# Performance work log

Measured on AMD Instinct MI355X. Metric: run time of the kernel, lower is better.

The kernel has to match this reference:

```python
import jax, jax.numpy as jnp
import numpy as np
import math

B, S, D = 4, 2048, 1024
H = 16
DH = D // H
NEG = -1e20


def setup_inputs() -> dict:
    key = jax.random.key(0)
    ks = jax.random.split(key, 8)
    Q_batch = jax.random.normal(ks[0], (B, S, D), dtype=jnp.float32)
    K_batch = jax.random.normal(ks[1], (B, S, D), dtype=jnp.float32)
    V_batch = jax.random.normal(ks[2], (B, S, D), dtype=jnp.float32)
    valid_lens = jax.random.randint(ks[3], (B,), 0, S).astype(jnp.int64)
    # LazyLinear weights, stored as (in, out) so projection is x @ W
    sc = 1.0 / math.sqrt(D)
    Wq = jax.random.normal(ks[4], (D, D), dtype=jnp.float32) * sc
    Wk = jax.random.normal(ks[5], (D, D), dtype=jnp.float32) * sc
    Wv = jax.random.normal(ks[6], (D, D), dtype=jnp.float32) * sc
    Wo = jax.random.normal(ks[7], (D, D), dtype=jnp.float32) * sc
    return {"Q_batch": Q_batch, "K_batch": K_batch, "V_batch": V_batch,
            "valid_lens": valid_lens, "Wq": Wq, "Wk": Wk, "Wv": Wv, "Wo": Wo}


def reference(Q_batch, K_batch, V_batch, valid_lens, Wq, Wk, Wv, Wo):
    b, nq, _ = Q_batch.shape
    nk = K_batch.shape[1]
    # project and split heads (feature dim split head-major, matching transpose_qkv)
    q = (Q_batch @ Wq).reshape(b, nq, H, DH).transpose(0, 2, 1, 3)  # (b,h,nq,dh)
    k = (K_batch @ Wk).reshape(b, nk, H, DH).transpose(0, 2, 1, 3)  # (b,h,nk,dh)
    v = (V_batch @ Wv).reshape(b, nk, H, DH).transpose(0, 2, 1, 3)  # (b,h,nk,dh)
    scores = jnp.einsum('bhqd,bhkd->bhqk', q, k) / math.sqrt(DH)
    # mask keys at position >= valid_lens[b] (shared across heads and queries)
    key_pos = jnp.arange(nk)
    mask = key_pos[None, None, None, :] < valid_lens[:, None, None, None]
    scores = jnp.where(mask, scores, NEG)
    w = jax.nn.softmax(scores, axis=-1)  # dropout rate 0 -> identity
    o = jnp.einsum('bhqk,bhkd->bhqd', w, v)           # (b,h,nq,dh)
    o = o.transpose(0, 2, 1, 3).reshape(b, nq, H * DH)  # concat heads
    return o @ Wo
```

## Files before the change

kernel.cpp:

```cpp
#include <hip/hip_runtime.h>
#include <stdint.h>

typedef unsigned short u16;
using bf16x8 = __attribute__((ext_vector_type(8))) __bf16;
using f32x4  = __attribute__((ext_vector_type(4))) float;
using u16x8  = __attribute__((ext_vector_type(8))) unsigned short;
using u16x4  = __attribute__((ext_vector_type(4))) unsigned short;

#define NH   16
#define DHD  64
#define SEQ  2048
#define DD   1024

__device__ inline u16 bfbits(float f) {
    __bf16 h = (__bf16)f;
    return __builtin_bit_cast(u16, h);
}

__device__ inline void gld16(const u16* g, u16* l) {
    __builtin_amdgcn_global_load_lds(
        (const __attribute__((address_space(1))) void*)g,
        (__attribute__((address_space(3))) void*)l,
        16, 0, 0);
}

__global__ __launch_bounds__(256) void transpose4(
    const float* __restrict__ s0, const float* __restrict__ s1,
    const float* __restrict__ s2, const float* __restrict__ s3,
    u16* __restrict__ d0, u16* __restrict__ d1,
    u16* __restrict__ d2, u16* __restrict__ d3)
{
    const float* src = s0; u16* dst = d0;
    if (blockIdx.z == 1) { src = s1; dst = d1; }
    else if (blockIdx.z == 2) { src = s2; dst = d2; }
    else if (blockIdx.z == 3) { src = s3; dst = d3; }

    __shared__ u16 tile[32][33];
    int tx = threadIdx.x, ty = threadIdx.y;
    int x = blockIdx.x * 32 + tx;
    int y0 = blockIdx.y * 32 + ty;
#pragma unroll
    for (int i = 0; i < 32; i += 8)
        tile[ty + i][tx] = bfbits(src[(size_t)(y0 + i) * DD + x]);
    __syncthreads();
    int x2 = blockIdx.y * 32 + tx;
    int y2 = blockIdx.x * 32 + ty;
#pragma unroll
    for (int i = 0; i < 32; i += 8)
        dst[(size_t)(y2 + i) * DD + x2] = tile[tx][ty + i];
}

__global__ __launch_bounds__(256) void cvt3(
    const float* __restrict__ s0, const float* __restrict__ s1,
    const float* __restrict__ s2,
    u16* __restrict__ d0, u16* __restrict__ d1, u16* __restrict__ d2,
    const int* __restrict__ vl)
{
    const float* src = s0; u16* dst = d0;
    if (blockIdx.z == 1) { src = s1; dst = d1; }
    else if (blockIdx.z == 2) { src = s2; dst = d2; }

    if (blockIdx.z != 0) {
        int r = blockIdx.x * 2;
        int v = vl[r >> 11];
        int ve = (v == 0) ? SEQ : v;
        int lim = ((ve + 127) >> 7) << 7;
        if ((r & (SEQ - 1)) >= lim) return;
    }

    size_t i = ((size_t)blockIdx.x * 256 + threadIdx.x) * 8;
    f32x4 a = *(const f32x4*)&src[i];
    f32x4 b = *(const f32x4*)&src[i + 4];
    u16x8 o;
#pragma unroll
    for (int j = 0; j < 4; ++j) { o[j] = bfbits(a[j]); o[j + 4] = bfbits(b[j]); }
    *(u16x8*)&dst[i] = o;
}

__global__ __launch_bounds__(256) void cvt1(
    const float* __restrict__ src, u16* __restrict__ dst)
{
    size_t i = ((size_t)blockIdx.x * 256 + threadIdx.x) * 8;
    f32x4 a = *(const f32x4*)&src[i];
    f32x4 b = *(const f32x4*)&src[i + 4];
    u16x8 o;
#pragma unroll
    for (int j = 0; j < 4; ++j) { o[j] = bfbits(a[j]); o[j + 4] = bfbits(b[j]); }
    *(u16x8*)&dst[i] = o;
}

template<int MODE>
__global__ __launch_bounds__(512, 4) void gemm_bt16(
    const u16* __restrict__ A0, const u16* __restrict__ A1, const u16* __restrict__ A2,
    const u16* __restrict__ B0, const u16* __restrict__ B1, const u16* __restrict__ B2,
    void* __restrict__ C0, void* __restrict__ C1, void* __restrict__ C2,
    const int* __restrict__ vl)
{
    const int K = 1024;
    const u16* A = A0; const u16* Bt = B0; void* C = C0;
    if (MODE == 3) {
        if (blockIdx.z == 1) { A = A1; Bt = B1; C = C1; }
        else if (blockIdx.z == 2) { A = A2; Bt = B2; C = C2; }
    }

    __shared__ __align__(16) u16 As[2][128 * 64];
    __shared__ __align__(16) u16 Bs[2][128 * 64];

    const int t = threadIdx.x;
    const int wave = t >> 6, lane = t & 63;
    const int l15 = lane & 15, q4 = lane >> 4;
    const int wm = (wave >> 1) * 32;
    const int wn = (wave & 1) * 64;

    const int gx = gridDim.x;
    const int nwg = gx * gridDim.y;
    int flat = blockIdx.y * gx + blockIdx.x;
    flat = (flat & 7) * (nwg >> 3) + (flat >> 3);
    const int m0 = (flat / gx) * 128, n0 = (flat % gx) * 128;

    if (MODE == 3 && blockIdx.z != 0) {
        int v = vl[m0 >> 11];
        int ve = (v == 0) ? SEQ : v;
        if ((m0 & (SEQ - 1)) >= ve) return;
    }

    const int sr = t >> 3;
    const int sg = (t & 7) ^ (sr & 7);
    const u16* gA = &A [(size_t)(m0 + sr) * K + sg * 8];
    const u16* gB = &Bt[(size_t)(n0 + sr) * K + sg * 8];
    const int ldst = sr * 64 + (t & 7) * 8;

    const int xr = (l15 & 7) * 8;

    f32x4 acc[2][4] = {};

    gld16(gA,                    &As[0][ldst]);
    gld16(gA + (size_t)64 * K,   &As[0][ldst + 4096]);
    gld16(gB,                    &Bs[0][ldst]);
    gld16(gB + (size_t)64 * K,   &Bs[0][ldst + 4096]);

    int cur = 0;
    for (int k0 = 0; k0 < K; k0 += 64) {
        __syncthreads();
        if (k0 + 64 < K) {
            const int nb = cur ^ 1;
            const size_t ko = k0 + 64;
            gld16(gA + ko,                  &As[nb][ldst]);
            gld16(gA + (size_t)64 * K + ko, &As[nb][ldst + 4096]);
            gld16(gB + ko,                  &Bs[nb][ldst]);
            gld16(gB + (size_t)64 * K + ko, &Bs[nb][ldst + 4096]);
        }

#pragma unroll
        for (int hf = 0; hf < 2; ++hf) {
            bf16x8 af[2], bfr[4];
#pragma unroll
            for (int i = 0; i < 2; ++i)
                af[i]  = *(const bf16x8*)&As[cur][(wm + i * 16 + l15) * 64 + ((hf * 32 + q4 * 8) ^ xr)];
#pragma unroll
            for (int j = 0; j < 4; ++j)
                bfr[j] = *(const bf16x8*)&Bs[cur][(wn + j * 16 + l15) * 64 + ((hf * 32 + q4 * 8) ^ xr)];
#pragma unroll
            for (int i = 0; i < 2; ++i)
#pragma unroll
                for (int j = 0; j < 4; ++j)
                    acc[i][j] = __builtin_amdgcn_mfma_f32_16x16x32_bf16(af[i], bfr[j], acc[i][j], 0, 0, 0);
        }
        cur ^= 1;
    }

    const bool vt_store = (MODE == 2) || (MODE == 3 && blockIdx.z == 2);

#pragma unroll
    for (int i = 0; i < 2; ++i) {
        int row_l = wm + i * 16 + q4 * 4;
#pragma unroll
        for (int j = 0; j < 4; ++j) {
            int col = n0 + wn + j * 16 + l15;
            if (MODE == 1) {
#pragma unroll
                for (int r = 0; r < 4; ++r) {
                    int row = m0 + row_l + r;
                    ((float*)C)[(size_t)row * DD + col] = acc[i][j][r];
                }
            } else if (vt_store) {
                int row = m0 + row_l;
                int b = row >> 11, s = row & (SEQ - 1);
                int h = col >> 6, dh = col & (DHD - 1);
                u16x4 pk;
#pragma unroll
                for (int r = 0; r < 4; ++r) pk[r] = bfbits(acc[i][j][r]);
                *(u16x4*)&((u16*)C)[(((size_t)(b * NH + h) * DHD + dh) << 11) | s] = pk;
            } else {
#pragma unroll
                for (int r = 0; r < 4; ++r) {
                    int row = m0 + row_l + r;
                    int b = row >> 11, s = row & (SEQ - 1);
                    int h = col >> 6, dh = col & (DHD - 1);
                    ((u16*)C)[(((size_t)(b * NH + h) * SEQ + s) << 6) | dh] = bfbits(acc[i][j][r]);
                }
            }
        }
    }
}

__global__ __launch_bounds__(256, 4) void attn(
    const u16* __restrict__ q_ws, const u16* __restrict__ k_ws,
    const u16* __restrict__ vT_ws, const int* __restrict__ valid_lens,
    u16* __restrict__ o_ws)
{
    const int bh = blockIdx.y;
    const int b = bh >> 4, h = bh & 15;
    const int qt = blockIdx.x;
    const int valid = valid_lens[b];
    const bool valid0 = (valid == 0);
    const int valid_eff = valid0 ? SEQ : valid;
    const int kt_n = (valid_eff + 63) >> 6;
    const float c2 = valid0 ? 0.f : 0.18033688011112042f;
    const float M2 = 17.312340490667562f;

    __shared__ __align__(16) u16 Kbuf[2][64 * 64];
    __shared__ __align__(16) u16 Vbuf[64 * 64];
    __shared__ __align__(16) u16 Ps[4][32][64];

    const int t = threadIdx.x;
    const int wave = t >> 6, lane = t & 63;
    const int l15 = lane & 15, q4 = lane >> 4;

    const size_t base  = (size_t)bh * SEQ * DHD;
    const size_t vbase = (size_t)bh * DHD * SEQ;

    const int q0 = qt * 128 + wave * 32;

    const int sr0 = wave * 16 + (lane >> 3);
    const int cg  = ((lane & 7) ^ (sr0 & 7)) * 8;
    const u16* gK = &k_ws [base  + (size_t)sr0 * DHD + cg];
    const u16* gV = &vT_ws[vbase + (size_t)sr0 * SEQ + cg];
    const int ldst = sr0 * 64 + (lane & 7) * 8;

    u16x8 ou;
#pragma unroll
    for (int j = 0; j < 8; ++j) ou[j] = 0x3F80;
    const bf16x8 ones = __builtin_bit_cast(bf16x8, ou);

    bf16x8 qf[2][2];
#pragma unroll
    for (int mi = 0; mi < 2; ++mi)
#pragma unroll
        for (int c = 0; c < 2; ++c)
            qf[mi][c] = *(const bf16x8*)&q_ws[base + (size_t)(q0 + mi * 16 + l15) * DHD + c * 32 + q4 * 8];

    f32x4 o4[2][4] = {};
    f32x4 l_acc[2] = {};

    const int swz  = (l15 & 7) * 8;

    gld16(gK,       &Kbuf[0][ldst]);
    gld16(gK + 512, &Kbuf[0][ldst + 512]);

    int cur = 0;
    for (int kt = 0; kt < kt_n; ++kt) {
        __syncthreads();
        {
            const u16* vv = gV + (size_t)kt * 64;
            gld16(vv,                   &Vbuf[ldst]);
            gld16(vv + (size_t)8 * SEQ, &Vbuf[ldst + 512]);
        }
        const bool pre = (kt + 1 < kt_n);
        if (pre) {
            const u16* kk = gK + (size_t)(kt + 1) * 64 * DHD;
            int bf = cur ^ 1;
            gld16(kk,       &Kbuf[bf][ldst]);
            gld16(kk + 512, &Kbuf[bf][ldst + 512]);
        }

        const u16* KK = Kbuf[cur];

        f32x4 s4[2][4] = {};
#pragma unroll
        for (int c = 0; c < 2; ++c)
#pragma unroll
            for (int ni = 0; ni < 4; ++ni) {
                bf16x8 kf = *(const bf16x8*)&KK[(ni * 16 + l15) * 64 + ((c * 32 + q4 * 8) ^ swz)];
#pragma unroll
                for (int mi = 0; mi < 2; ++mi)
                    s4[mi][ni] = __builtin_amdgcn_mfma_f32_16x16x32_bf16(kf, qf[mi][c], s4[mi][ni], 0, 0, 0);
            }

        const bool tile_full = valid0 || (kt * 64 + 64 <= valid_eff);
        if (tile_full) {
#pragma unroll
            for (int mi = 0; mi < 2; ++mi) {
                int qrow = mi * 16 + l15;
                int psw  = (l15 & 7) * 8;
#pragma unroll
                for (int ni = 0; ni < 4; ++ni) {
                    u16x4 pk;
#pragma unroll
                    for (int r = 0; r < 4; ++r) {
                        float p = __builtin_amdgcn_exp2f(__builtin_fmaf(s4[mi][ni][r], c2, -M2));
                        pk[r] = bfbits(p);
                    }
                    *(u16x4*)&Ps[wave][qrow][(ni * 16 + q4 * 4) ^ psw] = pk;
                }
            }
        } else {
#pragma unroll
            for (int mi = 0; mi < 2; ++mi) {
                int qrow = mi * 16 + l15;
                int psw  = (l15 & 7) * 8;
#pragma unroll
                for (int ni = 0; ni < 4; ++ni) {
                    u16x4 pk;
#pragma unroll
                    for (int r = 0; r < 4; ++r) {
                        bool ok = (kt * 64 + ni * 16 + q4 * 4 + r) < valid_eff;
                        float arg = ok ? __builtin_fmaf(s4[mi][ni][r], c2, -M2) : -1e30f;
                        pk[r] = bfbits(__builtin_amdgcn_exp2f(arg));
                    }
                    *(u16x4*)&Ps[wave][qrow][(ni * 16 + q4 * 4) ^ psw] = pk;
                }
            }
        }

        if (pre) asm volatile("s_waitcnt vmcnt(2)\n\ts_barrier" ::: "memory");
        else     asm volatile("s_waitcnt vmcnt(0)\n\ts_barrier" ::: "memory");

#pragma unroll
        for (int c = 0; c < 2; ++c) {
            bf16x8 pf[2];
#pragma unroll
            for (int mi = 0; mi < 2; ++mi) {
                pf[mi] = *(const bf16x8*)&Ps[wave][mi * 16 + l15][(c * 32 + q4 * 8) ^ ((l15 & 7) * 8)];
                l_acc[mi] = __builtin_amdgcn_mfma_f32_16x16x32_bf16(pf[mi], ones, l_acc[mi], 0, 0, 0);
            }
#pragma unroll
            for (int dt = 0; dt < 4; ++dt) {
                bf16x8 vf = *(const bf16x8*)&Vbuf[(dt * 16 + l15) * 64 + ((c * 32 + q4 * 8) ^ swz)];
#pragma unroll
                for (int mi = 0; mi < 2; ++mi)
                    o4[mi][dt] = __builtin_amdgcn_mfma_f32_16x16x32_bf16(pf[mi], vf, o4[mi][dt], 0, 0, 0);
            }
        }
        cur ^= 1;
    }

#pragma unroll
    for (int mi = 0; mi < 2; ++mi) {
        float inv[4];
#pragma unroll
        for (int r = 0; r < 4; ++r) inv[r] = 1.0f / l_acc[mi][r];
        int qrow = q0 + mi * 16 + q4 * 4;
#pragma unroll
        for (int dt = 0; dt < 4; ++dt) {
            int dh = dt * 16 + l15;
#pragma unroll
            for (int r = 0; r < 4; ++r) {
                float v = o4[mi][dt][r] * inv[r];
                o_ws[((size_t)(b * SEQ + qrow + r) << 10) | (h * DHD + dh)] = bfbits(v);
            }
        }
    }
}

extern "C" void kernel_launch(void* const* d_in, const int* in_sizes, int n_in,
                              void* d_out, int out_size, void* d_ws, size_t ws_size,
                              hipStream_t stream)
{
    (void)in_sizes; (void)n_in; (void)out_size;
    const float* Q  = (const float*)d_in[0];
    const float* Kb = (const float*)d_in[1];
    const float* V  = (const float*)d_in[2];
    const int*   vl = (const int*)d_in[3];
    const float* Wq = (const float*)d_in[4];
    const float* Wk = (const float*)d_in[5];
    const float* Wv = (const float*)d_in[6];
    const float* Wo = (const float*)d_in[7];
    float* out = (float*)d_out;

    char* ws = (char*)d_ws;
    u16* WqT   = (u16*)(ws + (size_t)0);
    u16* WkT   = (u16*)(ws + ((size_t)2 << 20));
    u16* WvT   = (u16*)(ws + ((size_t)4 << 20));
    u16* WoT   = (u16*)(ws + ((size_t)6 << 20));
    u16* q_ws  = (u16*)(ws + ((size_t)8 << 20));
    u16* k_ws  = (u16*)(ws + ((size_t)24 << 20));
    u16* vT_ws = (u16*)(ws + ((size_t)40 << 20));
    u16* o_ws  = (u16*)(ws + ((size_t)56 << 20));
    u16* Qbf   = (u16*)(ws + ((size_t)72 << 20));
    u16* Kbf   = (u16*)(ws + ((size_t)88 << 20));
    u16* Vbf   = (u16*)(ws + ((size_t)104 << 20));

    transpose4<<<dim3(32, 32, 4), dim3(32, 8), 0, stream>>>(
        Wq, Wk, Wv, Wo, WqT, WkT, WvT, WoT);

    const bool fused = ws_size >= ((size_t)120 << 20);
    if (fused) {
        cvt3<<<dim3(4096, 1, 3), 256, 0, stream>>>(Q, Kb, V, Qbf, Kbf, Vbf, vl);
        gemm_bt16<3><<<dim3(8, 64, 3), 512, 0, stream>>>(
            Qbf, Kbf, Vbf, WqT, WkT, WvT, q_ws, k_ws, vT_ws, vl);
    } else {
        cvt1<<<4096, 256, 0, stream>>>(Q, o_ws);
        gemm_bt16<0><<<dim3(8, 64), 512, 0, stream>>>(
            o_ws, nullptr, nullptr, WqT, nullptr, nullptr, q_ws, nullptr, nullptr, nullptr);
        cvt1<<<4096, 256, 0, stream>>>(Kb, o_ws);
        gemm_bt16<0><<<dim3(8, 64), 512, 0, stream>>>(
            o_ws, nullptr, nullptr, WkT, nullptr, nullptr, k_ws, nullptr, nullptr, nullptr);
        cvt1<<<4096, 256, 0, stream>>>(V, o_ws);
        gemm_bt16<2><<<dim3(8, 64), 512, 0, stream>>>(
            o_ws, nullptr, nullptr, WvT, nullptr, nullptr, vT_ws, nullptr, nullptr, nullptr);
    }

    attn<<<dim3(16, 64), 256, 0, stream>>>(q_ws, k_ws, vT_ws, vl, o_ws);

    gemm_bt16<1><<<dim3(8, 64), 512, 0, stream>>>(
        o_ws, nullptr, nullptr, WoT, nullptr, nullptr, out, nullptr, nullptr, nullptr);
}
```

Baseline: 283.2 us.

## Merge weight transpose into conversion kernel and double attention block size

Folds the four weight transposes into the input fp32-to-bf16 conversion launch as a fourth z-slice, removing one kernel launch in the fused path. The attention kernel now runs 512 threads (8 waves) per block covering 256 queries instead of 128, so each K/V tile loaded into shared memory is reused by twice as many query rows. Each thread issues one global-to-LDS load per tile instead of two, and the wait count is adjusted to match. The larger block doubles the P scratch in shared memory and halves the grid to 512 blocks, which may lower occupancy and make the load balance across varied valid lengths coarser.

```diff
diff --git a/kernel.cpp b/kernel.cpp
--- a/kernel.cpp
+++ b/kernel.cpp
@@ -24,6 +24,60 @@
         16, 0, 0);
 }
 
+__global__ __launch_bounds__(256) void prep(
+    const float* __restrict__ Q, const float* __restrict__ Kb,
+    const float* __restrict__ Vb,
+    const float* __restrict__ W0, const float* __restrict__ W1,
+    const float* __restrict__ W2, const float* __restrict__ W3,
+    u16* __restrict__ Qd, u16* __restrict__ Kd, u16* __restrict__ Vd,
+    u16* __restrict__ T0, u16* __restrict__ T1,
+    u16* __restrict__ T2, u16* __restrict__ T3,
+    const int* __restrict__ vl)
+{
+    const int z = blockIdx.z;
+    if (z == 3) {
+        const float* src = W0; u16* dst = T0;
+        int mat = blockIdx.x >> 10;
+        if (mat == 1) { src = W1; dst = T1; }
+        else if (mat == 2) { src = W2; dst = T2; }
+        else if (mat == 3) { src = W3; dst = T3; }
+        int wi = blockIdx.x & 1023;
+        int bx = wi & 31, by = wi >> 5;
+        __shared__ u16 tile[32][33];
+        int tx = threadIdx.x & 31, ty = threadIdx.x >> 5;
+        int x = bx * 32 + tx, y0 = by * 32 + ty;
+#pragma unroll
+        for (int i = 0; i < 32; i += 8)
+            tile[ty + i][tx] = bfbits(src[(size_t)(y0 + i) * DD + x]);
+        __syncthreads();
+        int x2 = by * 32 + tx, y2 = bx * 32 + ty;
+#pragma unroll
+        for (int i = 0; i < 32; i += 8)
+            dst[(size_t)(y2 + i) * DD + x2] = tile[tx][ty + i];
+        return;
+    }
+
+    const float* src = Q; u16* dst = Qd;
+    if (z == 1) { src = Kb; dst = Kd; }
+    else if (z == 2) { src = Vb; dst = Vd; }
+
+    if (z != 0) {
+        int r = blockIdx.x * 2;
+        int v = vl[r >> 11];
+        int ve = (v == 0) ? SEQ : v;
+        int lim = ((ve + 127) >> 7) << 7;
+        if ((r & (SEQ - 1)) >= lim) return;
+    }
+
+    size_t i = ((size_t)blockIdx.x * 256 + threadIdx.x) * 8;
+    f32x4 a = *(const f32x4*)&src[i];
+    f32x4 b = *(const f32x4*)&src[i + 4];
+    u16x8 o;
+#pragma unroll
+    for (int j = 0; j < 4; ++j) { o[j] = bfbits(a[j]); o[j + 4] = bfbits(b[j]); }
+    *(u16x8*)&dst[i] = o;
+}
+
 __global__ __launch_bounds__(256) void transpose4(
     const float* __restrict__ s0, const float* __restrict__ s1,
     const float* __restrict__ s2, const float* __restrict__ s3,
@@ -48,33 +102,6 @@
 #pragma unroll
     for (int i = 0; i < 32; i += 8)
         dst[(size_t)(y2 + i) * DD + x2] = tile[tx][ty + i];
-}
-
-__global__ __launch_bounds__(256) void cvt3(
-    const float* __restrict__ s0, const float* __restrict__ s1,
-    const float* __restrict__ s2,
-    u16* __restrict__ d0, u16* __restrict__ d1, u16* __restrict__ d2,
-    const int* __restrict__ vl)
-{
-    const float* src = s0; u16* dst = d0;
-    if (blockIdx.z == 1) { src = s1; dst = d1; }
-    else if (blockIdx.z == 2) { src = s2; dst = d2; }
-
-    if (blockIdx.z != 0) {
-        int r = blockIdx.x * 2;
-        int v = vl[r >> 11];
-        int ve = (v == 0) ? SEQ : v;
-        int lim = ((ve + 127) >> 7) << 7;
-        if ((r & (SEQ - 1)) >= lim) return;
-    }
-
-    size_t i = ((size_t)blockIdx.x * 256 + threadIdx.x) * 8;
-    f32x4 a = *(const f32x4*)&src[i];
-    f32x4 b = *(const f32x4*)&src[i + 4];
-    u16x8 o;
-#pragma unroll
-    for (int j = 0; j < 4; ++j) { o[j] = bfbits(a[j]); o[j + 4] = bfbits(b[j]); }
-    *(u16x8*)&dst[i] = o;
 }
 
 __global__ __launch_bounds__(256) void cvt1(
@@ -204,7 +231,7 @@
     }
 }
 
-__global__ __launch_bounds__(256, 4) void attn(
+__global__ __launch_bounds__(512, 4) void attn(
     const u16* __restrict__ q_ws, const u16* __restrict__ k_ws,
     const u16* __restrict__ vT_ws, const int* __restrict__ valid_lens,
     u16* __restrict__ o_ws)
@@ -221,7 +248,7 @@
 
     __shared__ __align__(16) u16 Kbuf[2][64 * 64];
     __shared__ __align__(16) u16 Vbuf[64 * 64];
-    __shared__ __align__(16) u16 Ps[4][32][64];
+    __shared__ __align__(16) u16 Ps[8][32][64];
 
     const int t = threadIdx.x;
     const int wave = t >> 6, lane = t & 63;
@@ -230,13 +257,13 @@
     const size_t base  = (size_t)bh * SEQ * DHD;
     const size_t vbase = (size_t)bh * DHD * SEQ;
 
-    const int q0 = qt * 128 + wave * 32;
-
-    const int sr0 = wave * 16 + (lane >> 3);
-    const int cg  = ((lane & 7) ^ (sr0 & 7)) * 8;
+    const int q0 = qt * 256 + wave * 32;
+
+    const int sr0 = t >> 3;
+    const int cg  = ((t & 7) ^ (sr0 & 7)) * 8;
     const u16* gK = &k_ws [base  + (size_t)sr0 * DHD + cg];
     const u16* gV = &vT_ws[vbase + (size_t)sr0 * SEQ + cg];
-    const int ldst = sr0 * 64 + (lane & 7) * 8;
+    const int ldst = sr0 * 64 + (t & 7) * 8;
 
     u16x8 ou;
 #pragma unroll
@@ -255,24 +282,15 @@
 
     const int swz  = (l15 & 7) * 8;
 
-    gld16(gK,       &Kbuf[0][ldst]);
-    gld16(gK + 512, &Kbuf[0][ldst + 512]);
+    gld16(gK, &Kbuf[0][ldst]);
 
     int cur = 0;
     for (int kt = 0; kt < kt_n; ++kt) {
         __syncthreads();
-        {
-            const u16* vv = gV + (size_t)kt * 64;
-            gld16(vv,                   &Vbuf[ldst]);
-            gld16(vv + (size_t)8 * SEQ, &Vbuf[ldst + 512]);
-        }
+        gld16(gV + (size_t)kt * 64, &Vbuf[ldst]);
         const bool pre = (kt + 1 < kt_n);
-        if (pre) {
-            const u16* kk = gK + (size_t)(kt + 1) * 64 * DHD;
-            int bf = cur ^ 1;
-            gld16(kk,       &Kbuf[bf][ldst]);
-            gld16(kk + 512, &Kbuf[bf][ldst + 512]);
-        }
+        if (pre)
+            gld16(gK + (size_t)(kt + 1) * 64 * DHD, &Kbuf[cur ^ 1][ldst]);
 
         const u16* KK = Kbuf[cur];
 
@@ -323,7 +341,7 @@
             }
         }
 
-        if (pre) asm volatile("s_waitcnt vmcnt(2)\n\ts_barrier" ::: "memory");
+        if (pre) asm volatile("s_waitcnt vmcnt(1)\n\ts_barrier" ::: "memory");
         else     asm volatile("s_waitcnt vmcnt(0)\n\ts_barrier" ::: "memory");
 
 #pragma unroll
@@ -391,15 +409,15 @@
     u16* Kbf   = (u16*)(ws + ((size_t)88 << 20));
     u16* Vbf   = (u16*)(ws + ((size_t)104 << 20));
 
-    transpose4<<<dim3(32, 32, 4), dim3(32, 8), 0, stream>>>(
-        Wq, Wk, Wv, Wo, WqT, WkT, WvT, WoT);
-
     const bool fused = ws_size >= ((size_t)120 << 20);
     if (fused) {
-        cvt3<<<dim3(4096, 1, 3), 256, 0, stream>>>(Q, Kb, V, Qbf, Kbf, Vbf, vl);
+        prep<<<dim3(4096, 1, 4), 256, 0, stream>>>(
+            Q, Kb, V, Wq, Wk, Wv, Wo, Qbf, Kbf, Vbf, WqT, WkT, WvT, WoT, vl);
         gemm_bt16<3><<<dim3(8, 64, 3), 512, 0, stream>>>(
             Qbf, Kbf, Vbf, WqT, WkT, WvT, q_ws, k_ws, vT_ws, vl);
     } else {
+        transpose4<<<dim3(32, 32, 4), dim3(32, 8), 0, stream>>>(
+            Wq, Wk, Wv, Wo, WqT, WkT, WvT, WoT);
         cvt1<<<4096, 256, 0, stream>>>(Q, o_ws);
         gemm_bt16<0><<<dim3(8, 64), 512, 0, stream>>>(
             o_ws, nullptr, nullptr, WqT, nullptr, nullptr, q_ws, nullptr, nullptr, nullptr);
@@ -411,7 +429,7 @@
             o_ws, nullptr, nullptr, WvT, nullptr, nullptr, vT_ws, nullptr, nullptr, nullptr);
     }
 
-    attn<<<dim3(16, 64), 256, 0, stream>>>(q_ws, k_ws, vT_ws, vl, o_ws);
+    attn<<<dim3(8, 64), 512, 0, stream>>>(q_ws, k_ws, vT_ws, vl, o_ws);
 
     gemm_bt16<1><<<dim3(8, 64), 512, 0, stream>>>(
         o_ws, nullptr, nullptr, WoT, nullptr, nullptr, out, nullptr, nullptr, nullptr);
```

Result: no change. 281.6 us (-0.6%).

## Fuse fp32-to-bf16 input conversion into the QKV projection GEMM A-tile load

Applied to the files above, without the earlier changes.

Removes the separate cvt3 pass and its bf16 staging buffers. The MODE 3 GEMM now loads fp32 activations directly into registers, converts them to bf16, and writes them into swizzled LDS after the MFMA loop, which overlaps the next tile's global loads with compute. This saves a full write and re-read of the bf16 copies, but the A operand now reads twice the bytes per tile through registers instead of direct-to-LDS loads. It also adds register pressure and sched barriers.

```diff
diff --git a/kernel.cpp b/kernel.cpp
--- a/kernel.cpp
+++ b/kernel.cpp
@@ -50,33 +50,6 @@
         dst[(size_t)(y2 + i) * DD + x2] = tile[tx][ty + i];
 }
 
-__global__ __launch_bounds__(256) void cvt3(
-    const float* __restrict__ s0, const float* __restrict__ s1,
-    const float* __restrict__ s2,
-    u16* __restrict__ d0, u16* __restrict__ d1, u16* __restrict__ d2,
-    const int* __restrict__ vl)
-{
-    const float* src = s0; u16* dst = d0;
-    if (blockIdx.z == 1) { src = s1; dst = d1; }
-    else if (blockIdx.z == 2) { src = s2; dst = d2; }
-
-    if (blockIdx.z != 0) {
-        int r = blockIdx.x * 2;
-        int v = vl[r >> 11];
-        int ve = (v == 0) ? SEQ : v;
-        int lim = ((ve + 127) >> 7) << 7;
-        if ((r & (SEQ - 1)) >= lim) return;
-    }
-
-    size_t i = ((size_t)blockIdx.x * 256 + threadIdx.x) * 8;
-    f32x4 a = *(const f32x4*)&src[i];
-    f32x4 b = *(const f32x4*)&src[i + 4];
-    u16x8 o;
-#pragma unroll
-    for (int j = 0; j < 4; ++j) { o[j] = bfbits(a[j]); o[j + 4] = bfbits(b[j]); }
-    *(u16x8*)&dst[i] = o;
-}
-
 __global__ __launch_bounds__(256) void cvt1(
     const float* __restrict__ src, u16* __restrict__ dst)
 {
@@ -96,6 +69,7 @@
     void* __restrict__ C0, void* __restrict__ C1, void* __restrict__ C2,
     const int* __restrict__ vl)
 {
+    constexpr bool ACVT = (MODE == 3);
     const int K = 1024;
     const u16* A = A0; const u16* Bt = B0; void* C = C0;
     if (MODE == 3) {
@@ -126,30 +100,60 @@
 
     const int sr = t >> 3;
     const int sg = (t & 7) ^ (sr & 7);
-    const u16* gA = &A [(size_t)(m0 + sr) * K + sg * 8];
     const u16* gB = &Bt[(size_t)(n0 + sr) * K + sg * 8];
     const int ldst = sr * 64 + (t & 7) * 8;
 
+    const int arow = t >> 2;
+    const int acol = (t & 3) * 16;
+    const int asw  = (arow & 7) * 8;
+    const float* gAf = nullptr;
+    const u16*   gA  = nullptr;
+    if constexpr (ACVT) gAf = &((const float*)A)[(size_t)(m0 + arow) * K + acol];
+    else                gA  = &A[(size_t)(m0 + sr) * K + sg * 8];
+
     const int xr = (l15 & 7) * 8;
 
     f32x4 acc[2][4] = {};
-
-    gld16(gA,                    &As[0][ldst]);
-    gld16(gA + (size_t)64 * K,   &As[0][ldst + 4096]);
-    gld16(gB,                    &Bs[0][ldst]);
-    gld16(gB + (size_t)64 * K,   &Bs[0][ldst + 4096]);
+    f32x4 ar[4];
+
+    if constexpr (ACVT) {
+#pragma unroll
+        for (int j = 0; j < 4; ++j) ar[j] = *(const f32x4*)(gAf + 4 * j);
+    } else {
+        gld16(gA,                  &As[0][ldst]);
+        gld16(gA + (size_t)64 * K, &As[0][ldst + 4096]);
+    }
+    gld16(gB,                  &Bs[0][ldst]);
+    gld16(gB + (size_t)64 * K, &Bs[0][ldst + 4096]);
+    if constexpr (ACVT) {
+        u16x8 w0, w1;
+#pragma unroll
+        for (int j = 0; j < 4; ++j) {
+            w0[j] = bfbits(ar[0][j]); w0[j + 4] = bfbits(ar[1][j]);
+            w1[j] = bfbits(ar[2][j]); w1[j + 4] = bfbits(ar[3][j]);
+        }
+        *(u16x8*)&As[0][arow * 64 + (acol ^ asw)]       = w0;
+        *(u16x8*)&As[0][arow * 64 + ((acol + 8) ^ asw)] = w1;
+    }
 
     int cur = 0;
     for (int k0 = 0; k0 < K; k0 += 64) {
         __syncthreads();
-        if (k0 + 64 < K) {
+        const bool pre = (k0 + 64 < K);
+        if (pre) {
             const int nb = cur ^ 1;
             const size_t ko = k0 + 64;
-            gld16(gA + ko,                  &As[nb][ldst]);
-            gld16(gA + (size_t)64 * K + ko, &As[nb][ldst + 4096]);
+            if constexpr (ACVT) {
+#pragma unroll
+                for (int j = 0; j < 4; ++j) ar[j] = *(const f32x4*)(gAf + ko + 4 * j);
+            } else {
+                gld16(gA + ko,                  &As[nb][ldst]);
+                gld16(gA + (size_t)64 * K + ko, &As[nb][ldst + 4096]);
+            }
             gld16(gB + ko,                  &Bs[nb][ldst]);
             gld16(gB + (size_t)64 * K + ko, &Bs[nb][ldst + 4096]);
         }
+        __builtin_amdgcn_sched_barrier(0);
 
 #pragma unroll
         for (int hf = 0; hf < 2; ++hf) {
@@ -165,6 +169,19 @@
 #pragma unroll
                 for (int j = 0; j < 4; ++j)
                     acc[i][j] = __builtin_amdgcn_mfma_f32_16x16x32_bf16(af[i], bfr[j], acc[i][j], 0, 0, 0);
+        }
+        __builtin_amdgcn_sched_barrier(0);
+
+        if (ACVT && pre) {
+            const int nb = cur ^ 1;
+            u16x8 w0, w1;
+#pragma unroll
+            for (int j = 0; j < 4; ++j) {
+                w0[j] = bfbits(ar[0][j]); w0[j + 4] = bfbits(ar[1][j]);
+                w1[j] = bfbits(ar[2][j]); w1[j + 4] = bfbits(ar[3][j]);
+            }
+            *(u16x8*)&As[nb][arow * 64 + (acol ^ asw)]       = w0;
+            *(u16x8*)&As[nb][arow * 64 + ((acol + 8) ^ asw)] = w1;
         }
         cur ^= 1;
     }
@@ -387,18 +404,15 @@
     u16* k_ws  = (u16*)(ws + ((size_t)24 << 20));
     u16* vT_ws = (u16*)(ws + ((size_t)40 << 20));
     u16* o_ws  = (u16*)(ws + ((size_t)56 << 20));
-    u16* Qbf   = (u16*)(ws + ((size_t)72 << 20));
-    u16* Kbf   = (u16*)(ws + ((size_t)88 << 20));
-    u16* Vbf   = (u16*)(ws + ((size_t)104 << 20));
 
     transpose4<<<dim3(32, 32, 4), dim3(32, 8), 0, stream>>>(
         Wq, Wk, Wv, Wo, WqT, WkT, WvT, WoT);
 
     const bool fused = ws_size >= ((size_t)120 << 20);
     if (fused) {
-        cvt3<<<dim3(4096, 1, 3), 256, 0, stream>>>(Q, Kb, V, Qbf, Kbf, Vbf, vl);
         gemm_bt16<3><<<dim3(8, 64, 3), 512, 0, stream>>>(
-            Qbf, Kbf, Vbf, WqT, WkT, WvT, q_ws, k_ws, vT_ws, vl);
+            (const u16*)Q, (const u16*)Kb, (const u16*)V,
+            WqT, WkT, WvT, q_ws, k_ws, vT_ws, vl);
     } else {
         cvt1<<<4096, 256, 0, stream>>>(Q, o_ws);
         gemm_bt16<0><<<dim3(8, 64), 512, 0, stream>>>(
```

Result: slower. 313.6 us (+10.7%).
